# Kernel optimization log

Hardware: AMD Instinct MI355X
Metric: run time of the kernel (lower is better)

## Reference

```python
import jax, jax.numpy as jnp
import numpy as np

B, H, S, D = 4, 16, 2048, 64

def setup_inputs() -> dict:
    key = jax.random.key(0)
    kq, kk, kv = jax.random.split(key, 3)
    q = jax.random.normal(kq, (B, H, S, D), dtype=jnp.float32)
    k = jax.random.normal(kk, (B, H, S, D), dtype=jnp.float32)
    v = jax.random.normal(kv, (B, H, S, D), dtype=jnp.float32)
    # causal mask: True where attention is DISALLOWED (masked_fill semantics)
    row = jnp.arange(S)[:, None]
    col = jnp.arange(S)[None, :]
    attn_mask = (col > row)[None, None, :, :]  # [1,1,S,S] bool
    return {"q": q, "k": k, "v": v, "attn_mask": attn_mask}

def reference(q, k, v, attn_mask):
    scale = 1.0 / jnp.sqrt(jnp.float32(q.shape[-1]))
    # [B,H,S,S] scores
    scores = jnp.einsum("bhqd,bhkd->bhqk", q, k) * scale
    scores = jnp.where(attn_mask, -jnp.inf, scores)
    attn = jax.nn.softmax(scores, axis=-1)
    # dropout p=0 (eval) -> identity
    context = jnp.einsum("bhqk,bhkd->bhqd", attn, v)
    return context
```

## Files before the change

### kernel.cpp

```cpp
#include <hip/hip_runtime.h>

#define BB 4
#define HH 16
#define SS 2048
#define DD 64

typedef __bf16 bf16x8 __attribute__((ext_vector_type(8)));
typedef float  f32x4  __attribute__((ext_vector_type(4)));
typedef unsigned short u16;
typedef unsigned int   u32;
typedef unsigned int   u32x2 __attribute__((ext_vector_type(2)));

__device__ __forceinline__ u32 pack2bf(float a, float b) {
    u32 r;
    asm("v_cvt_pk_bf16_f32 %0, %1, %2" : "=v"(r) : "v"(a), "v"(b));
    return r;
}

__device__ __forceinline__ u32x2 pl32(u32 a, u32 b) {
#if __has_builtin(__builtin_amdgcn_permlane32_swap)
    return __builtin_amdgcn_permlane32_swap(a, b, false, false);
#else
    asm("v_permlane32_swap_b32 %0, %1" : "+v"(a), "+v"(b));
    u32x2 r; r.x = a; r.y = b; return r;
#endif
}
__device__ __forceinline__ u32x2 pl16(u32 a, u32 b) {
#if __has_builtin(__builtin_amdgcn_permlane16_swap)
    return __builtin_amdgcn_permlane16_swap(a, b, false, false);
#else
    asm("v_permlane16_swap_b32 %0, %1" : "+v"(a), "+v"(b));
    u32x2 r; r.x = a; r.y = b; return r;
#endif
}

template<bool DOU>
__device__ __forceinline__ void fa_tile(
    const char* __restrict__ Bb, const int kv0,
    const bf16x8 (&qf)[2][2],
    const int s0L, const int s0U,
    const int m16, const int quad, const int offA0, const int offA1,
    const bf16x8 ones,
    f32x4 (&accL)[4], f32x4 (&accU)[4], f32x4 &laccL, f32x4 &laccU)
{
    const f32x4 vzero = {0.f, 0.f, 0.f, 0.f};
    u32 ppL[4][2], ppU[4][2];
    #pragma unroll
    for (int st = 0; st < 4; ++st) {
        const bf16x8 kf0 = *(const bf16x8*)(Bb + st * 2048 + offA0);
        const bf16x8 kf1 = *(const bf16x8*)(Bb + st * 2048 + offA1);
        {
            f32x4 s = __builtin_amdgcn_mfma_f32_16x16x32_bf16(
                kf0, qf[0][0], vzero, 0, 0, 0);
            s = __builtin_amdgcn_mfma_f32_16x16x32_bf16(
                kf1, qf[0][1], s, 0, 0, 0);
            if (kv0 + 63 > s0L) {
                const int qq = s0L + m16;
                const int kb = kv0 + st * 16 + quad * 4;
                #pragma unroll
                for (int r = 0; r < 4; ++r)
                    if (kb + r > qq) s[r] = -1e30f;
            }
            const float p0 = __builtin_exp2f(s[0]);
            const float p1 = __builtin_exp2f(s[1]);
            const float p2 = __builtin_exp2f(s[2]);
            const float p3 = __builtin_exp2f(s[3]);
            ppL[st][0] = pack2bf(p0, p1);
            ppL[st][1] = pack2bf(p2, p3);
        }
        if (DOU) {
            f32x4 s = __builtin_amdgcn_mfma_f32_16x16x32_bf16(
                kf0, qf[1][0], vzero, 0, 0, 0);
            s = __builtin_amdgcn_mfma_f32_16x16x32_bf16(
                kf1, qf[1][1], s, 0, 0, 0);
            if (kv0 + 63 > s0U) {
                const int qq = s0U + m16;
                const int kb = kv0 + st * 16 + quad * 4;
                #pragma unroll
                for (int r = 0; r < 4; ++r)
                    if (kb + r > qq) s[r] = -1e30f;
            }
            const float p0 = __builtin_exp2f(s[0]);
            const float p1 = __builtin_exp2f(s[1]);
            const float p2 = __builtin_exp2f(s[2]);
            const float p3 = __builtin_exp2f(s[3]);
            ppU[st][0] = pack2bf(p0, p1);
            ppU[st][1] = pack2bf(p2, p3);
        }
    }
    bf16x8 pfL[2], pfU[2];
    #pragma unroll
    for (int kc = 0; kc < 2; ++kc) {
        u32x2 t0 = pl32(ppL[2 * kc][0], ppL[2 * kc + 1][0]);
        u32x2 r0 = pl16(t0.x, t0.y);
        u32x2 t1 = pl32(ppL[2 * kc][1], ppL[2 * kc + 1][1]);
        u32x2 r1 = pl16(t1.x, t1.y);
        union { u32 u[4]; bf16x8 v; } pfu;
        pfu.u[0] = r0.x; pfu.u[1] = r1.x;
        pfu.u[2] = r0.y; pfu.u[3] = r1.y;
        pfL[kc] = pfu.v;
    }
    if (DOU) {
        #pragma unroll
        for (int kc = 0; kc < 2; ++kc) {
            u32x2 t0 = pl32(ppU[2 * kc][0], ppU[2 * kc + 1][0]);
            u32x2 r0 = pl16(t0.x, t0.y);
            u32x2 t1 = pl32(ppU[2 * kc][1], ppU[2 * kc + 1][1]);
            u32x2 r1 = pl16(t1.x, t1.y);
            union { u32 u[4]; bf16x8 v; } pfu;
            pfu.u[0] = r0.x; pfu.u[1] = r1.x;
            pfu.u[2] = r0.y; pfu.u[3] = r1.y;
            pfU[kc] = pfu.v;
        }
    }
    laccL = __builtin_amdgcn_mfma_f32_16x16x32_bf16(ones, pfL[0], laccL, 0, 0, 0);
    laccL = __builtin_amdgcn_mfma_f32_16x16x32_bf16(ones, pfL[1], laccL, 0, 0, 0);
    if (DOU) {
        laccU = __builtin_amdgcn_mfma_f32_16x16x32_bf16(ones, pfU[0], laccU, 0, 0, 0);
        laccU = __builtin_amdgcn_mfma_f32_16x16x32_bf16(ones, pfU[1], laccU, 0, 0, 0);
    }
    #pragma unroll
    for (int dt = 0; dt < 4; ++dt) {
        const bf16x8 vf0 = *(const bf16x8*)(Bb + 8192 + dt * 2048 + offA0);
        const bf16x8 vf1 = *(const bf16x8*)(Bb + 8192 + dt * 2048 + offA1);
        accL[dt] = __builtin_amdgcn_mfma_f32_16x16x32_bf16(
            vf0, pfL[0], accL[dt], 0, 0, 0);
        accL[dt] = __builtin_amdgcn_mfma_f32_16x16x32_bf16(
            vf1, pfL[1], accL[dt], 0, 0, 0);
        if (DOU) {
            accU[dt] = __builtin_amdgcn_mfma_f32_16x16x32_bf16(
                vf0, pfU[0], accU[dt], 0, 0, 0);
            accU[dt] = __builtin_amdgcn_mfma_f32_16x16x32_bf16(
                vf1, pfU[1], accU[dt], 0, 0, 0);
        }
    }
}

__global__ __launch_bounds__(512, 4) void fa3(
    const float* __restrict__ q, const float* __restrict__ kg,
    const float* __restrict__ vg, float* __restrict__ out)
{
    const int tid  = threadIdx.x;
    const int lane = tid & 63;
    const int w    = tid >> 6;
    const int quad = lane >> 4;
    const int m16  = lane & 15;
    const int bx   = blockIdx.x;
    const int rr   = bx >> 8;
    const int jj   = (bx >> 6) & 3;
    const int bh   = bx & 63;
    const int a    = rr ? (7 - jj) : jj;
    const size_t base = (size_t)bh * SS * DD;
    const int s0U = a * 128 + w * 16;
    const int s0L = (15 - a) * 128 + w * 16;

    __shared__ __align__(16) u16 KV[2][8192];

    const bool isK = (tid < 256);
    const int  h   = tid & 255;
    const int  kr  = h >> 2;
    const int  kc  = h & 3;
    const int  vs4 = (h >> 4) * 4;
    const int  vd4 = (h & 15) * 4;
    const float* gK = kg + base + (size_t)kr * DD + kc * 16;
    const float* gV = vg + base + (size_t)vs4 * DD + vd4;

    const int swz   = (m16 & 7) << 4;
    const int offA0 = m16 * 128 + ((quad * 16) ^ swz);
    const int offA1 = m16 * 128 + ((quad * 16 + 64) ^ swz);

    const float qsc = 0.18033688011112042f;
    bf16x8 qf[2][2];
    #pragma unroll
    for (int sx = 0; sx < 2; ++sx) {
        const int s0 = sx ? s0U : s0L;
        #pragma unroll
        for (int dc = 0; dc < 2; ++dc) {
            const float* qp = q + base + (size_t)(s0 + m16) * DD
                              + dc * 32 + quad * 8;
            float4 fa = *(const float4*)(qp);
            float4 fb = *(const float4*)(qp + 4);
            union { u32 u[4]; bf16x8 v; } t;
            t.u[0] = pack2bf(fa.x * qsc, fa.y * qsc);
            t.u[1] = pack2bf(fa.z * qsc, fa.w * qsc);
            t.u[2] = pack2bf(fb.x * qsc, fb.y * qsc);
            t.u[3] = pack2bf(fb.z * qsc, fb.w * qsc);
            qf[sx][dc] = t.v;
        }
    }

    const f32x4 vzero = {0.f, 0.f, 0.f, 0.f};
    f32x4 accL[4], accU[4], laccL = vzero, laccU = vzero;
    #pragma unroll
    for (int dt = 0; dt < 4; ++dt) { accL[dt] = vzero; accU[dt] = vzero; }

    union { u32 u[4]; bf16x8 v; } onesu;
    onesu.u[0] = 0x3F803F80u; onesu.u[1] = 0x3F803F80u;
    onesu.u[2] = 0x3F803F80u; onesu.u[3] = 0x3F803F80u;
    const bf16x8 ones = onesu.v;

    const int ntiles = 32 - 2 * a;

    auto gload = [&](int tt, float4& x0, float4& x1, float4& x2, float4& x3) {
        if (isK) {
            const float4* p = (const float4*)(gK + (size_t)tt * 4096);
            x0 = p[0]; x1 = p[1]; x2 = p[2]; x3 = p[3];
        } else {
            const float* p = gV + (size_t)tt * 4096;
            x0 = *(const float4*)(p);
            x1 = *(const float4*)(p + DD);
            x2 = *(const float4*)(p + 2 * DD);
            x3 = *(const float4*)(p + 3 * DD);
        }
    };
    auto cvt_write = [&](int buf, float4 x0, float4 x1, float4 x2, float4 x3) {
        if (isK) {
            uint4 A, B;
            A.x = pack2bf(x0.x, x0.y); A.y = pack2bf(x0.z, x0.w);
            A.z = pack2bf(x1.x, x1.y); A.w = pack2bf(x1.z, x1.w);
            B.x = pack2bf(x2.x, x2.y); B.y = pack2bf(x2.z, x2.w);
            B.z = pack2bf(x3.x, x3.y); B.w = pack2bf(x3.z, x3.w);
            u16* kd = &KV[buf][kr * 64];
            *(uint4*)(kd + (((2 * kc)     ^ (kr & 7)) << 3)) = A;
            *(uint4*)(kd + (((2 * kc + 1) ^ (kr & 7)) << 3)) = B;
        } else {
            const float c0[4] = {x0.x, x0.y, x0.z, x0.w};
            const float c1[4] = {x1.x, x1.y, x1.z, x1.w};
            const float c2[4] = {x2.x, x2.y, x2.z, x2.w};
            const float c3[4] = {x3.x, x3.y, x3.z, x3.w};
            #pragma unroll
            for (int j = 0; j < 4; ++j) {
                uint2 o;
                o.x = pack2bf(c0[j], c1[j]);
                o.y = pack2bf(c2[j], c3[j]);
                const int row = vd4 + j;
                *(uint2*)(&KV[buf][4096 + row * 64 +
                    (((vs4 >> 3) ^ (row & 7)) << 3) + (vs4 & 4)]) = o;
            }
        }
    };

    {
        float4 x0, x1, x2, x3;
        gload(0, x0, x1, x2, x3);
        cvt_write(0, x0, x1, x2, x3);
    }

    for (int t = 0; t < ntiles; ++t) {
        __syncthreads();
        const int kv0 = t * 64;
        const char* Bb = (const char*)&KV[t & 1][0];

        float4 x0, x1, x2, x3;
        const bool hn = (t + 1 < ntiles);
        if (hn) gload(t + 1, x0, x1, x2, x3);

        const bool doL = (kv0 <= s0L + 15);
        const bool doU = (kv0 <= s0U + 15);
        if (doL) {
            if (doU)
                fa_tile<true >(Bb, kv0, qf, s0L, s0U, m16, quad, offA0, offA1,
                               ones, accL, accU, laccL, laccU);
            else
                fa_tile<false>(Bb, kv0, qf, s0L, s0U, m16, quad, offA0, offA1,
                               ones, accL, accU, laccL, laccU);
        }

        if (hn) cvt_write((t + 1) & 1, x0, x1, x2, x3);
    }

    {
        const float inv = 1.f / laccL[0];
        const int qq = s0L + m16;
        #pragma unroll
        for (int dt = 0; dt < 4; ++dt) {
            float4 o = make_float4(accL[dt][0] * inv, accL[dt][1] * inv,
                                   accL[dt][2] * inv, accL[dt][3] * inv);
            *(float4*)(out + base + (size_t)qq * DD + dt * 16 + quad * 4) = o;
        }
    }
    {
        const float inv = 1.f / laccU[0];
        const int qq = s0U + m16;
        #pragma unroll
        for (int dt = 0; dt < 4; ++dt) {
            float4 o = make_float4(accU[dt][0] * inv, accU[dt][1] * inv,
                                   accU[dt][2] * inv, accU[dt][3] * inv);
            *(float4*)(out + base + (size_t)qq * DD + dt * 16 + quad * 4) = o;
        }
    }
}

extern "C" void kernel_launch(void* const* d_in, const int* in_sizes, int n_in,
                              void* d_out, int out_size, void* d_ws, size_t ws_size,
                              hipStream_t stream)
{
    const float* q = (const float*)d_in[0];
    const float* k = (const float*)d_in[1];
    const float* v = (const float*)d_in[2];
    float* out = (float*)d_out;
    (void)d_ws; (void)ws_size;

    fa3<<<dim3(8 * 64), dim3(512), 0, stream>>>(q, k, v, out);
}
```

Baseline: 195.9 us.

## Split paired causal query blocks into separate workgroups with heavy-first ordering

Each workgroup used to process two 128-row query blocks (a light one and its mirrored heavy one) so that causal work was balanced. Now each workgroup handles a single query block, the grid doubles to 1024 blocks, and blocks are ordered heaviest first. Register use per thread roughly halves, so launch bounds request 8 waves per SIMD. The LDS swizzle also changes to an XOR pattern that depends on more row bits, with separate offsets for even and odd sub-tiles, to cut bank conflicts. The cost is that every K/V tile is loaded and converted once per query block instead of being shared by two, which adds global traffic and conversion work.

```diff
diff --git a/kernel.cpp b/kernel.cpp
--- a/kernel.cpp
+++ b/kernel.cpp
@@ -34,109 +34,7 @@
 #endif
 }
 
-template<bool DOU>
-__device__ __forceinline__ void fa_tile(
-    const char* __restrict__ Bb, const int kv0,
-    const bf16x8 (&qf)[2][2],
-    const int s0L, const int s0U,
-    const int m16, const int quad, const int offA0, const int offA1,
-    const bf16x8 ones,
-    f32x4 (&accL)[4], f32x4 (&accU)[4], f32x4 &laccL, f32x4 &laccU)
-{
-    const f32x4 vzero = {0.f, 0.f, 0.f, 0.f};
-    u32 ppL[4][2], ppU[4][2];
-    #pragma unroll
-    for (int st = 0; st < 4; ++st) {
-        const bf16x8 kf0 = *(const bf16x8*)(Bb + st * 2048 + offA0);
-        const bf16x8 kf1 = *(const bf16x8*)(Bb + st * 2048 + offA1);
-        {
-            f32x4 s = __builtin_amdgcn_mfma_f32_16x16x32_bf16(
-                kf0, qf[0][0], vzero, 0, 0, 0);
-            s = __builtin_amdgcn_mfma_f32_16x16x32_bf16(
-                kf1, qf[0][1], s, 0, 0, 0);
-            if (kv0 + 63 > s0L) {
-                const int qq = s0L + m16;
-                const int kb = kv0 + st * 16 + quad * 4;
-                #pragma unroll
-                for (int r = 0; r < 4; ++r)
-                    if (kb + r > qq) s[r] = -1e30f;
-            }
-            const float p0 = __builtin_exp2f(s[0]);
-            const float p1 = __builtin_exp2f(s[1]);
-            const float p2 = __builtin_exp2f(s[2]);
-            const float p3 = __builtin_exp2f(s[3]);
-            ppL[st][0] = pack2bf(p0, p1);
-            ppL[st][1] = pack2bf(p2, p3);
-        }
-        if (DOU) {
-            f32x4 s = __builtin_amdgcn_mfma_f32_16x16x32_bf16(
-                kf0, qf[1][0], vzero, 0, 0, 0);
-            s = __builtin_amdgcn_mfma_f32_16x16x32_bf16(
-                kf1, qf[1][1], s, 0, 0, 0);
-            if (kv0 + 63 > s0U) {
-                const int qq = s0U + m16;
-                const int kb = kv0 + st * 16 + quad * 4;
-                #pragma unroll
-                for (int r = 0; r < 4; ++r)
-                    if (kb + r > qq) s[r] = -1e30f;
-            }
-            const float p0 = __builtin_exp2f(s[0]);
-            const float p1 = __builtin_exp2f(s[1]);
-            const float p2 = __builtin_exp2f(s[2]);
-            const float p3 = __builtin_exp2f(s[3]);
-            ppU[st][0] = pack2bf(p0, p1);
-            ppU[st][1] = pack2bf(p2, p3);
-        }
-    }
-    bf16x8 pfL[2], pfU[2];
-    #pragma unroll
-    for (int kc = 0; kc < 2; ++kc) {
-        u32x2 t0 = pl32(ppL[2 * kc][0], ppL[2 * kc + 1][0]);
-        u32x2 r0 = pl16(t0.x, t0.y);
-        u32x2 t1 = pl32(ppL[2 * kc][1], ppL[2 * kc + 1][1]);
-        u32x2 r1 = pl16(t1.x, t1.y);
-        union { u32 u[4]; bf16x8 v; } pfu;
-        pfu.u[0] = r0.x; pfu.u[1] = r1.x;
-        pfu.u[2] = r0.y; pfu.u[3] = r1.y;
-        pfL[kc] = pfu.v;
-    }
-    if (DOU) {
-        #pragma unroll
-        for (int kc = 0; kc < 2; ++kc) {
-            u32x2 t0 = pl32(ppU[2 * kc][0], ppU[2 * kc + 1][0]);
-            u32x2 r0 = pl16(t0.x, t0.y);
-            u32x2 t1 = pl32(ppU[2 * kc][1], ppU[2 * kc + 1][1]);
-            u32x2 r1 = pl16(t1.x, t1.y);
-            union { u32 u[4]; bf16x8 v; } pfu;
-            pfu.u[0] = r0.x; pfu.u[1] = r1.x;
-            pfu.u[2] = r0.y; pfu.u[3] = r1.y;
-            pfU[kc] = pfu.v;
-        }
-    }
-    laccL = __builtin_amdgcn_mfma_f32_16x16x32_bf16(ones, pfL[0], laccL, 0, 0, 0);
-    laccL = __builtin_amdgcn_mfma_f32_16x16x32_bf16(ones, pfL[1], laccL, 0, 0, 0);
-    if (DOU) {
-        laccU = __builtin_amdgcn_mfma_f32_16x16x32_bf16(ones, pfU[0], laccU, 0, 0, 0);
-        laccU = __builtin_amdgcn_mfma_f32_16x16x32_bf16(ones, pfU[1], laccU, 0, 0, 0);
-    }
-    #pragma unroll
-    for (int dt = 0; dt < 4; ++dt) {
-        const bf16x8 vf0 = *(const bf16x8*)(Bb + 8192 + dt * 2048 + offA0);
-        const bf16x8 vf1 = *(const bf16x8*)(Bb + 8192 + dt * 2048 + offA1);
-        accL[dt] = __builtin_amdgcn_mfma_f32_16x16x32_bf16(
-            vf0, pfL[0], accL[dt], 0, 0, 0);
-        accL[dt] = __builtin_amdgcn_mfma_f32_16x16x32_bf16(
-            vf1, pfL[1], accL[dt], 0, 0, 0);
-        if (DOU) {
-            accU[dt] = __builtin_amdgcn_mfma_f32_16x16x32_bf16(
-                vf0, pfU[0], accU[dt], 0, 0, 0);
-            accU[dt] = __builtin_amdgcn_mfma_f32_16x16x32_bf16(
-                vf1, pfU[1], accU[dt], 0, 0, 0);
-        }
-    }
-}
-
-__global__ __launch_bounds__(512, 4) void fa3(
+__global__ __launch_bounds__(512, 8) void fa3(
     const float* __restrict__ q, const float* __restrict__ kg,
     const float* __restrict__ vg, float* __restrict__ out)
 {
@@ -147,12 +45,16 @@
     const int m16  = lane & 15;
     const int bx   = blockIdx.x;
     const int rr   = bx >> 8;
-    const int jj   = (bx >> 6) & 3;
-    const int bh   = bx & 63;
-    const int a    = rr ? (7 - jj) : jj;
+    const int cc   = bx & 255;
+    const int jj   = cc >> 6;
+    const int bh   = cc & 63;
+    int qblk;
+    if      (rr == 0) qblk = 15 - jj;
+    else if (rr == 1) qblk = 8 + jj;
+    else if (rr == 2) qblk = 7 - jj;
+    else              qblk = jj;
     const size_t base = (size_t)bh * SS * DD;
-    const int s0U = a * 128 + w * 16;
-    const int s0L = (15 - a) * 128 + w * 16;
+    const int s0 = qblk * 128 + w * 16;
 
     __shared__ __align__(16) u16 KV[2][8192];
 
@@ -165,41 +67,38 @@
     const float* gK = kg + base + (size_t)kr * DD + kc * 16;
     const float* gV = vg + base + (size_t)vs4 * DD + vd4;
 
-    const int swz   = (m16 & 7) << 4;
-    const int offA0 = m16 * 128 + ((quad * 16) ^ swz);
-    const int offA1 = m16 * 128 + ((quad * 16 + 64) ^ swz);
+    const int cxe   = (m16 & 7) ^ ((m16 >> 3) & 3);
+    const int offE0 = m16 * 128 + ((quad ^ cxe) << 4);
+    const int offE1 = m16 * 128 + (((quad + 4) ^ cxe) << 4);
+    const int offO0 = offE0 ^ 32;
+    const int offO1 = offE1 ^ 32;
 
     const float qsc = 0.18033688011112042f;
-    bf16x8 qf[2][2];
+    bf16x8 qf[2];
     #pragma unroll
-    for (int sx = 0; sx < 2; ++sx) {
-        const int s0 = sx ? s0U : s0L;
-        #pragma unroll
-        for (int dc = 0; dc < 2; ++dc) {
-            const float* qp = q + base + (size_t)(s0 + m16) * DD
-                              + dc * 32 + quad * 8;
-            float4 fa = *(const float4*)(qp);
-            float4 fb = *(const float4*)(qp + 4);
-            union { u32 u[4]; bf16x8 v; } t;
-            t.u[0] = pack2bf(fa.x * qsc, fa.y * qsc);
-            t.u[1] = pack2bf(fa.z * qsc, fa.w * qsc);
-            t.u[2] = pack2bf(fb.x * qsc, fb.y * qsc);
-            t.u[3] = pack2bf(fb.z * qsc, fb.w * qsc);
-            qf[sx][dc] = t.v;
-        }
+    for (int dc = 0; dc < 2; ++dc) {
+        const float* qp = q + base + (size_t)(s0 + m16) * DD + dc * 32 + quad * 8;
+        float4 fa = *(const float4*)(qp);
+        float4 fb = *(const float4*)(qp + 4);
+        union { u32 u[4]; bf16x8 v; } t;
+        t.u[0] = pack2bf(fa.x * qsc, fa.y * qsc);
+        t.u[1] = pack2bf(fa.z * qsc, fa.w * qsc);
+        t.u[2] = pack2bf(fb.x * qsc, fb.y * qsc);
+        t.u[3] = pack2bf(fb.z * qsc, fb.w * qsc);
+        qf[dc] = t.v;
     }
 
     const f32x4 vzero = {0.f, 0.f, 0.f, 0.f};
-    f32x4 accL[4], accU[4], laccL = vzero, laccU = vzero;
+    f32x4 acc[4], lacc = vzero;
     #pragma unroll
-    for (int dt = 0; dt < 4; ++dt) { accL[dt] = vzero; accU[dt] = vzero; }
+    for (int dt = 0; dt < 4; ++dt) acc[dt] = vzero;
 
     union { u32 u[4]; bf16x8 v; } onesu;
     onesu.u[0] = 0x3F803F80u; onesu.u[1] = 0x3F803F80u;
     onesu.u[2] = 0x3F803F80u; onesu.u[3] = 0x3F803F80u;
     const bf16x8 ones = onesu.v;
 
-    const int ntiles = 32 - 2 * a;
+    const int ntiles = 2 * qblk + 2;
 
     auto gload = [&](int tt, float4& x0, float4& x1, float4& x2, float4& x3) {
         if (isK) {
@@ -220,9 +119,10 @@
             A.z = pack2bf(x1.x, x1.y); A.w = pack2bf(x1.z, x1.w);
             B.x = pack2bf(x2.x, x2.y); B.y = pack2bf(x2.z, x2.w);
             B.z = pack2bf(x3.x, x3.y); B.w = pack2bf(x3.z, x3.w);
+            const int kx = (kr & 7) ^ ((kr >> 3) & 3);
             u16* kd = &KV[buf][kr * 64];
-            *(uint4*)(kd + (((2 * kc)     ^ (kr & 7)) << 3)) = A;
-            *(uint4*)(kd + (((2 * kc + 1) ^ (kr & 7)) << 3)) = B;
+            *(uint4*)(kd + (((2 * kc)     ^ kx) << 3)) = A;
+            *(uint4*)(kd + (((2 * kc + 1) ^ kx) << 3)) = B;
         } else {
             const float c0[4] = {x0.x, x0.y, x0.z, x0.w};
             const float c1[4] = {x1.x, x1.y, x1.z, x1.w};
@@ -234,8 +134,9 @@
                 o.x = pack2bf(c0[j], c1[j]);
                 o.y = pack2bf(c2[j], c3[j]);
                 const int row = vd4 + j;
+                const int vx  = (row & 7) ^ ((row >> 3) & 3);
                 *(uint2*)(&KV[buf][4096 + row * 64 +
-                    (((vs4 >> 3) ^ (row & 7)) << 3) + (vs4 & 4)]) = o;
+                    (((vs4 >> 3) ^ vx) << 3) + (vs4 & 4)]) = o;
             }
         }
     };
@@ -255,39 +156,69 @@
         const bool hn = (t + 1 < ntiles);
         if (hn) gload(t + 1, x0, x1, x2, x3);
 
-        const bool doL = (kv0 <= s0L + 15);
-        const bool doU = (kv0 <= s0U + 15);
-        if (doL) {
-            if (doU)
-                fa_tile<true >(Bb, kv0, qf, s0L, s0U, m16, quad, offA0, offA1,
-                               ones, accL, accU, laccL, laccU);
-            else
-                fa_tile<false>(Bb, kv0, qf, s0L, s0U, m16, quad, offA0, offA1,
-                               ones, accL, accU, laccL, laccU);
+        if (kv0 <= s0 + 15) {
+            u32 pp[4][2];
+            #pragma unroll
+            for (int st = 0; st < 4; ++st) {
+                const int o0 = (st & 1) ? offO0 : offE0;
+                const int o1 = (st & 1) ? offO1 : offE1;
+                const bf16x8 kf0 = *(const bf16x8*)(Bb + st * 2048 + o0);
+                const bf16x8 kf1 = *(const bf16x8*)(Bb + st * 2048 + o1);
+                f32x4 s = __builtin_amdgcn_mfma_f32_16x16x32_bf16(
+                    kf0, qf[0], vzero, 0, 0, 0);
+                s = __builtin_amdgcn_mfma_f32_16x16x32_bf16(
+                    kf1, qf[1], s, 0, 0, 0);
+                if (kv0 + 63 > s0) {
+                    const int qq = s0 + m16;
+                    const int kb = kv0 + st * 16 + quad * 4;
+                    #pragma unroll
+                    for (int r = 0; r < 4; ++r)
+                        if (kb + r > qq) s[r] = -1e30f;
+                }
+                const float p0 = __builtin_exp2f(s[0]);
+                const float p1 = __builtin_exp2f(s[1]);
+                const float p2 = __builtin_exp2f(s[2]);
+                const float p3 = __builtin_exp2f(s[3]);
+                pp[st][0] = pack2bf(p0, p1);
+                pp[st][1] = pack2bf(p2, p3);
+            }
+            bf16x8 pf[2];
+            #pragma unroll
+            for (int kk = 0; kk < 2; ++kk) {
+                u32x2 t0 = pl32(pp[2 * kk][0], pp[2 * kk + 1][0]);
+                u32x2 r0 = pl16(t0.x, t0.y);
+                u32x2 t1 = pl32(pp[2 * kk][1], pp[2 * kk + 1][1]);
+                u32x2 r1 = pl16(t1.x, t1.y);
+                union { u32 u[4]; bf16x8 v; } pfu;
+                pfu.u[0] = r0.x; pfu.u[1] = r1.x;
+                pfu.u[2] = r0.y; pfu.u[3] = r1.y;
+                pf[kk] = pfu.v;
+            }
+            lacc = __builtin_amdgcn_mfma_f32_16x16x32_bf16(ones, pf[0], lacc, 0, 0, 0);
+            lacc = __builtin_amdgcn_mfma_f32_16x16x32_bf16(ones, pf[1], lacc, 0, 0, 0);
+            #pragma unroll
+            for (int dt = 0; dt < 4; ++dt) {
+                const int o0 = (dt & 1) ? offO0 : offE0;
+                const int o1 = (dt & 1) ? offO1 : offE1;
+                const bf16x8 vf0 = *(const bf16x8*)(Bb + 8192 + dt * 2048 + o0);
+                const bf16x8 vf1 = *(const bf16x8*)(Bb + 8192 + dt * 2048 + o1);
+                acc[dt] = __builtin_amdgcn_mfma_f32_16x16x32_bf16(
+                    vf0, pf[0], acc[dt], 0, 0, 0);
+                acc[dt] = __builtin_amdgcn_mfma_f32_16x16x32_bf16(
+                    vf1, pf[1], acc[dt], 0, 0, 0);
+            }
         }
 
         if (hn) cvt_write((t + 1) & 1, x0, x1, x2, x3);
     }
 
-    {
-        const float inv = 1.f / laccL[0];
-        const int qq = s0L + m16;
-        #pragma unroll
-        for (int dt = 0; dt < 4; ++dt) {
-            float4 o = make_float4(accL[dt][0] * inv, accL[dt][1] * inv,
-                                   accL[dt][2] * inv, accL[dt][3] * inv);
-            *(float4*)(out + base + (size_t)qq * DD + dt * 16 + quad * 4) = o;
-        }
-    }
-    {
-        const float inv = 1.f / laccU[0];
-        const int qq = s0U + m16;
-        #pragma unroll
-        for (int dt = 0; dt < 4; ++dt) {
-            float4 o = make_float4(accU[dt][0] * inv, accU[dt][1] * inv,
-                                   accU[dt][2] * inv, accU[dt][3] * inv);
-            *(float4*)(out + base + (size_t)qq * DD + dt * 16 + quad * 4) = o;
-        }
+    const float inv = 1.f / lacc[0];
+    const int qq = s0 + m16;
+    #pragma unroll
+    for (int dt = 0; dt < 4; ++dt) {
+        float4 o = make_float4(acc[dt][0] * inv, acc[dt][1] * inv,
+                               acc[dt][2] * inv, acc[dt][3] * inv);
+        *(float4*)(out + base + (size_t)qq * DD + dt * 16 + quad * 4) = o;
     }
 }
 
@@ -301,5 +232,5 @@
     float* out = (float*)d_out;
     (void)d_ws; (void)ws_size;
 
-    fa3<<<dim3(8 * 64), dim3(512), 0, stream>>>(q, k, v, out);
-}
+    fa3<<<dim3(16 * 64), dim3(512), 0, stream>>>(q, k, v, out);
+}
```

Result: slower. 405.3 us (+106.9%).
